# Kernel tuning notes

Measured on AMD Instinct MI355X. Metric: run time of the kernel, lower is better.

## Reference

```python
import jax, jax.numpy as jnp
import numpy as np

B, S, D_IN, D_OUT = 2, 2048, 2048, 2048
NH, NKV = 16, 4
HD = D_OUT // NH          # 128
GS = NH // NKV            # 4


def _rope_tables(seq_len, head_dim, base=10000.0):
    inv = 1.0 / (base ** (np.arange(0, head_dim, 2, dtype=np.float32) / head_dim))
    t = np.arange(seq_len, dtype=np.float32)
    ang = np.outer(t, inv)                       # [S, HD/2]
    ang = np.concatenate([ang, ang], axis=-1)    # [S, HD]
    return jnp.asarray(np.cos(ang)), jnp.asarray(np.sin(ang))


def setup_inputs() -> dict:
    key = jax.random.key(0)
    ks = jax.random.split(key, 5)
    x = jax.random.normal(ks[0], (B, S, D_IN), dtype=jnp.float32)
    Wq = jax.random.normal(ks[1], (D_IN, D_OUT), dtype=jnp.float32) * 0.02
    Wk = jax.random.normal(ks[2], (D_IN, NKV * HD), dtype=jnp.float32) * 0.02
    Wv = jax.random.normal(ks[3], (D_IN, NKV * HD), dtype=jnp.float32) * 0.02
    Wo = jax.random.normal(ks[4], (D_OUT, D_OUT), dtype=jnp.float32) * 0.02
    cos, sin = _rope_tables(S, HD)
    return {"x": x, "Wq": Wq, "Wk": Wk, "Wv": Wv, "Wo": Wo, "cos": cos, "sin": sin}


def _apply_rope(t, cos, sin):
    # t: [b, h, s, hd]; cos/sin: [s, hd]
    hd = t.shape[-1]
    t1, t2 = t[..., : hd // 2], t[..., hd // 2:]
    rot = jnp.concatenate([-t2, t1], axis=-1)
    return t * cos[None, None, :, :] + rot * sin[None, None, :, :]


def reference(x, Wq, Wk, Wv, Wo, cos, sin):
    b, s, _ = x.shape
    q = (x @ Wq).reshape(b, s, NH, HD).transpose(0, 2, 1, 3)    # [b, nh, s, hd]
    k = (x @ Wk).reshape(b, s, NKV, HD).transpose(0, 2, 1, 3)   # [b, nkv, s, hd]
    v = (x @ Wv).reshape(b, s, NKV, HD).transpose(0, 2, 1, 3)
    q = _apply_rope(q, cos, sin)
    k = _apply_rope(k, cos, sin)
    # GQA: repeat_interleave kv heads to match query heads
    k = jnp.repeat(k, GS, axis=1)                               # [b, nh, s, hd]
    v = jnp.repeat(v, GS, axis=1)
    att = jnp.einsum("bhqd,bhkd->bhqk", q, k) / jnp.sqrt(jnp.float32(HD))
    causal = jnp.triu(jnp.ones((s, s), dtype=bool), k=1)         # True above diag
    att = jnp.where(causal[None, None, :, :], -jnp.inf, att)
    att = jax.nn.softmax(att, axis=-1)
    ctx = jnp.einsum("bhqk,bhkd->bhqd", att, v)                  # [b, nh, s, hd]
    ctx = ctx.transpose(0, 2, 1, 3).reshape(b, s, NH * HD)
    return ctx @ Wo
```

## Files before the change

kernel.cpp:

```cpp
#include <hip/hip_runtime.h>

#define B_ 2
#define S_ 2048
#define DIN 2048
#define DOUT 2048
#define NH 16
#define NKV 4
#define HD 128
#define QS3 3072
#define KOFF 2048
#define VOFF 2560
#define SMAX 14.0f
#define NQT 16

typedef __bf16 bf16x8 __attribute__((ext_vector_type(8)));
typedef float f32x4 __attribute__((ext_vector_type(4)));

__device__ inline unsigned short f2bf(float f) {
  union { float f; unsigned int u; } v; v.f = f;
  unsigned int r = v.u + 0x7fffu + ((v.u >> 16) & 1u);
  return (unsigned short)(r >> 16);
}
__device__ inline unsigned short f2bf_trunc(float f) {
  return (unsigned short)(__builtin_bit_cast(unsigned int, f) >> 16);
}
__device__ inline float bf2f(unsigned short h) {
  union { unsigned int u; float f; } v; v.u = ((unsigned int)h) << 16;
  return v.f;
}
#if __has_builtin(__builtin_amdgcn_exp2f)
__device__ inline float exp2_fast(float x) { return __builtin_amdgcn_exp2f(x); }
#else
__device__ inline float exp2_fast(float x) {
  float r;
  asm("v_exp_f32 %0, %1\n\ts_nop 1" : "=v"(r) : "v"(x));
  return r;
}
#endif

__device__ inline void gl_lds16(const void* g, void* l) {
  __builtin_amdgcn_global_load_lds(
      (const __attribute__((address_space(1))) void*)g,
      (__attribute__((address_space(3))) void*)l, 16, 0, 0);
}

template <int N>
__device__ inline float rrot(float v) {
  return __builtin_bit_cast(float,
      __builtin_amdgcn_update_dpp(0, __builtin_bit_cast(int, v), 0x120 | N, 0xF, 0xF, true));
}
__device__ inline float rsum16(float v) {
  v += rrot<1>(v); v += rrot<2>(v); v += rrot<4>(v); v += rrot<8>(v);
  return v;
}

__global__ __launch_bounds__(256) void cast_bf16_k(const float* __restrict__ in,
                                                   unsigned short* __restrict__ out, int n4) {
  int i = blockIdx.x * 256 + threadIdx.x;
  if (i >= n4) return;
  float4 v = ((const float4*)in)[i];
  ushort4 o;
  o.x = f2bf(v.x); o.y = f2bf(v.y); o.z = f2bf(v.z); o.w = f2bf(v.w);
  ((ushort4*)out)[i] = o;
}

__global__ void transpose_cast_k(const float* __restrict__ W, unsigned short* __restrict__ Wt,
                                 int K, int N, float scale) {
  __shared__ float tile[32][33];
  int n0 = blockIdx.x * 32, k0 = blockIdx.y * 32;
  int tx = threadIdx.x, ty = threadIdx.y;
  #pragma unroll
  for (int j = 0; j < 32; j += 8)
    tile[ty + j][tx] = W[(size_t)(k0 + ty + j) * N + n0 + tx];
  __syncthreads();
  #pragma unroll
  for (int j = 0; j < 32; j += 8)
    Wt[(size_t)(n0 + ty + j) * K + k0 + tx] = f2bf(tile[tx][ty + j] * scale);
}

__global__ void transpose_v_k(const unsigned short* __restrict__ QKV,
                              unsigned short* __restrict__ Vt) {
  __shared__ unsigned short t[32][33];
  int c0 = blockIdx.x * 32, s0 = blockIdx.y * 32, b = blockIdx.z;
  int tx = threadIdx.x, ty = threadIdx.y;
  #pragma unroll
  for (int j = 0; j < 32; j += 8)
    t[ty + j][tx] = QKV[(size_t)(b * S_ + s0 + ty + j) * QS3 + VOFF + c0 + tx];
  __syncthreads();
  #pragma unroll
  for (int j = 0; j < 32; j += 8)
    Vt[(size_t)(b * (NKV * HD) + c0 + ty + j) * S_ + s0 + tx] = t[tx][ty + j];
}

template <int OUT_BF16>
__global__ __launch_bounds__(256) void gemm_bt_k(const unsigned short* __restrict__ A,
                                                 const unsigned short* __restrict__ Bt,
                                                 void* __restrict__ Cout,
                                                 int M, int N, int K) {
  __shared__ unsigned short As[128 * 32];
  __shared__ unsigned short Bs[128 * 32];
  int tid = threadIdx.x;
  int lane = tid & 63, wave = tid >> 6;
  int wy = wave >> 1, wx = wave & 1;
  int rowA0 = blockIdx.x * 128, rowB0 = blockIdx.y * 128;
  int m16 = lane & 15, quad = lane >> 4;
  int xq = (m16 >> 1) & 3;
  f32x4 acc[4][4] = {};

  int r0 = tid >> 2, l0 = (tid & 3) ^ ((r0 >> 1) & 3);
  int c1 = 256 + tid;
  int r1 = c1 >> 2, l1 = (c1 & 3) ^ ((r1 >> 1) & 3);
  const unsigned short* pa0 = A  + (size_t)(rowA0 + r0) * K + l0 * 8;
  const unsigned short* pa1 = A  + (size_t)(rowA0 + r1) * K + l1 * 8;
  const unsigned short* pb0 = Bt + (size_t)(rowB0 + r0) * K + l0 * 8;
  const unsigned short* pb1 = Bt + (size_t)(rowB0 + r1) * K + l1 * 8;
  unsigned short* la = As + (tid & 192) * 8;
  unsigned short* lb = Bs + (tid & 192) * 8;

  for (int k0 = 0; k0 < K; k0 += 32) {
    __syncthreads();
    gl_lds16(pa0 + k0, la);
    gl_lds16(pb0 + k0, lb);
    gl_lds16(pa1 + k0, la + 2048);
    gl_lds16(pb1 + k0, lb + 2048);
    __syncthreads();
    bf16x8 af[4], bfr[4];
    #pragma unroll
    for (int i = 0; i < 4; ++i)
      af[i] = *(const bf16x8*)(As + (wy * 64 + i * 16 + m16) * 32 + (quad ^ xq) * 8);
    #pragma unroll
    for (int j = 0; j < 4; ++j)
      bfr[j] = *(const bf16x8*)(Bs + (wx * 64 + j * 16 + m16) * 32 + (quad ^ xq) * 8);
    #pragma unroll
    for (int i = 0; i < 4; ++i)
      #pragma unroll
      for (int j = 0; j < 4; ++j)
        acc[i][j] = __builtin_amdgcn_mfma_f32_16x16x32_bf16(af[i], bfr[j], acc[i][j], 0, 0, 0);
  }

  #pragma unroll
  for (int i = 0; i < 4; ++i) {
    #pragma unroll
    for (int j = 0; j < 4; ++j) {
      int row = rowA0 + wy * 64 + i * 16 + quad * 4;
      int col = rowB0 + wx * 64 + j * 16 + m16;
      #pragma unroll
      for (int r = 0; r < 4; ++r) {
        float v = acc[i][j][r];
        if (OUT_BF16)
          ((unsigned short*)Cout)[(size_t)(row + r) * N + col] = f2bf(v);
        else
          ((float*)Cout)[(size_t)(row + r) * N + col] = v;
      }
    }
  }
}

__global__ __launch_bounds__(256) void rope_k(unsigned short* __restrict__ T,
                                              const float* __restrict__ cosT,
                                              const float* __restrict__ sinT,
                                              int stride, int off, int lognh) {
  int idx = blockIdx.x * 256 + threadIdx.x;
  int d = (idx & 15) * 4;
  int t = idx >> 4;
  int nh = 1 << lognh;
  int h = t & (nh - 1);
  int bs = t >> lognh;
  int s = bs & (S_ - 1);
  unsigned short* p = T + (size_t)bs * stride + off + h * HD;
  ushort4 a = *(ushort4*)(p + d);
  ushort4 bq = *(ushort4*)(p + 64 + d);
  float4 c = *(const float4*)(cosT + s * HD + d);
  float4 sn = *(const float4*)(sinT + s * HD + d);
  ushort4 o1, o2;
  o1.x = f2bf(bf2f(a.x) * c.x - bf2f(bq.x) * sn.x);
  o2.x = f2bf(bf2f(bq.x) * c.x + bf2f(a.x) * sn.x);
  o1.y = f2bf(bf2f(a.y) * c.y - bf2f(bq.y) * sn.y);
  o2.y = f2bf(bf2f(bq.y) * c.y + bf2f(a.y) * sn.y);
  o1.z = f2bf(bf2f(a.z) * c.z - bf2f(bq.z) * sn.z);
  o2.z = f2bf(bf2f(bq.z) * c.z + bf2f(a.z) * sn.z);
  o1.w = f2bf(bf2f(a.w) * c.w - bf2f(bq.w) * sn.w);
  o2.w = f2bf(bf2f(bq.w) * c.w + bf2f(a.w) * sn.w);
  *(ushort4*)(p + d) = o1;
  *(ushort4*)(p + 64 + d) = o2;
}

#define LDP 40
__global__ __launch_bounds__(256) void flash_k(const unsigned short* __restrict__ QKV,
                                               const unsigned short* __restrict__ Vt,
                                               unsigned short* __restrict__ ctx,
                                               unsigned short* __restrict__ Opart,
                                               float* __restrict__ lpart,
                                               int CHUNK, int units_per_bh) {
  __shared__ unsigned short Ks4[4][32 * 128];
  __shared__ unsigned short Vs4[4][128 * 32];
  __shared__ unsigned short Ps[4][32 * LDP];
  int tid = threadIdx.x;
  int lane = tid & 63, w = tid >> 6;
  int m16 = lane & 15, quad = lane >> 4;
  int h = blockIdx.y, b = blockIdx.z;
  int g = h >> 2;

  int u = units_per_bh - 1 - (int)blockIdx.x;
  int qt = 0, prefix = 0, nc = 1;
  for (qt = 0; qt < NQT; ++qt) {
    nc = ((qt + 1) * 128 + CHUNK - 1) / CHUNK;
    if (prefix + nc > u) break;
    prefix += nc;
  }
  int ci = u - prefix;
  bool sole = (nc == 1);
  int kbeg = ci * CHUNK;
  int kend = min(kbeg + CHUNK, (qt + 1) * 128);
  int ntiles = (kend - kbeg) >> 5;
  int unit = (b * NH + h) * units_per_bh + u;

  bf16x8 qf[2][4];
  #pragma unroll
  for (int m = 0; m < 2; ++m) {
    int qrow = qt * 128 + w * 32 + m * 16 + m16;
    const unsigned short* Qp = QKV + (size_t)(b * S_ + qrow) * QS3 + h * HD;
    #pragma unroll
    for (int c = 0; c < 4; ++c) qf[m][c] = *(const bf16x8*)(Qp + c * 32 + quad * 8);
  }

  f32x4 o[2][8] = {};
  float lp[2][4] = {};

  int kxq = m16 & 7;
  int vxq = (m16 >> 1) & 3;

  int krow0 = tid >> 4, kcl0 = (tid & 15) ^ (krow0 & 7);
  int kc1 = 256 + tid;
  int krow1 = kc1 >> 4, kcl1 = (kc1 & 15) ^ (krow1 & 7);
  const unsigned short* kg0 = QKV + (size_t)(b * S_ + krow0) * QS3 + KOFF + g * HD + kcl0 * 8;
  const unsigned short* kg1 = QKV + (size_t)(b * S_ + krow1) * QS3 + KOFF + g * HD + kcl1 * 8;
  int vhd0 = tid >> 2, vcl0 = (tid & 3) ^ ((vhd0 >> 1) & 3);
  int vc1 = 256 + tid;
  int vhd1 = vc1 >> 2, vcl1 = (vc1 & 3) ^ ((vhd1 >> 1) & 3);
  const unsigned short* vg0 = Vt + (size_t)((b * NKV + g) * HD + vhd0) * S_ + vcl0 * 8;
  const unsigned short* vg1 = Vt + (size_t)((b * NKV + g) * HD + vhd1) * S_ + vcl1 * 8;
  int ldsoff = (tid & 192) * 8;
  unsigned short* pw = &Ps[w][0];

  auto stage = [&](int t) {
    int kb = kbeg + t * 32;
    int sl = t & 3;
    gl_lds16(kg0 + (size_t)kb * QS3, Ks4[sl] + ldsoff);
    gl_lds16(kg1 + (size_t)kb * QS3, Ks4[sl] + ldsoff + 2048);
    gl_lds16(vg0 + kb, Vs4[sl] + ldsoff);
    gl_lds16(vg1 + kb, Vs4[sl] + ldsoff + 2048);
  };

  auto qk_tile = [&](const unsigned short* ks, f32x4 (&sf)[2][2]) {
    #pragma unroll
    for (int c = 0; c < 4; ++c)
      #pragma unroll
      for (int f = 0; f < 2; ++f) {
        bf16x8 kf = *(const bf16x8*)(ks + (f * 16 + m16) * 128 + ((c * 4 + quad) ^ kxq) * 8);
        sf[0][f] = __builtin_amdgcn_mfma_f32_16x16x32_bf16(qf[0][c], kf, sf[0][f], 0, 0, 0);
        sf[1][f] = __builtin_amdgcn_mfma_f32_16x16x32_bf16(qf[1][c], kf, sf[1][f], 0, 0, 0);
      }
  };

  auto sm_pv = [&](f32x4 (&sf)[2][2], int kb, const unsigned short* vs) {
    #pragma unroll
    for (int m = 0; m < 2; ++m) {
      int base = qt * 128 + w * 32 + m * 16;
      bool nm = (kb + 31 > base);
      #pragma unroll
      for (int r = 0; r < 4; ++r) {
        float s0 = sf[m][0][r], s1 = sf[m][1][r];
        if (nm) {
          int qr = base + quad * 4 + r;
          if (kb + m16 > qr)      s0 = -1e30f;
          if (kb + 16 + m16 > qr) s1 = -1e30f;
        }
        float p0 = exp2_fast(s0 - SMAX);
        float p1 = exp2_fast(s1 - SMAX);
        lp[m][r] += p0 + p1;
        pw[(m * 16 + quad * 4 + r) * LDP + m16]      = f2bf_trunc(p0);
        pw[(m * 16 + quad * 4 + r) * LDP + 16 + m16] = f2bf_trunc(p1);
      }
    }
    bf16x8 pa0 = *(const bf16x8*)(pw + m16 * LDP + quad * 8);
    bf16x8 pa1 = *(const bf16x8*)(pw + (16 + m16) * LDP + quad * 8);
    #pragma unroll
    for (int nt = 0; nt < 8; ++nt) {
      bf16x8 vf = *(const bf16x8*)(vs + (nt * 16 + m16) * 32 + (quad ^ vxq) * 8);
      o[0][nt] = __builtin_amdgcn_mfma_f32_16x16x32_bf16(pa0, vf, o[0][nt], 0, 0, 0);
      o[1][nt] = __builtin_amdgcn_mfma_f32_16x16x32_bf16(pa1, vf, o[1][nt], 0, 0, 0);
    }
  };

  stage(0);
  stage(1);

  for (int tp = 0; tp < ntiles; tp += 2) {
    __syncthreads();
    if (tp + 2 < ntiles) { stage(tp + 2); stage(tp + 3); }
    int sa = tp & 3, sb = (tp + 1) & 3;
    f32x4 sfa[2][2] = {}, sfb[2][2] = {};
    qk_tile(Ks4[sa], sfa);
    qk_tile(Ks4[sb], sfb);
    sm_pv(sfa, kbeg + tp * 32, Vs4[sa]);
    sm_pv(sfb, kbeg + tp * 32 + 32, Vs4[sb]);
  }

  if (sole) {
    #pragma unroll
    for (int m = 0; m < 2; ++m)
      #pragma unroll
      for (int r = 0; r < 4; ++r) {
        float inv = 1.f / rsum16(lp[m][r]);
        int row = qt * 128 + w * 32 + m * 16 + quad * 4 + r;
        #pragma unroll
        for (int nt = 0; nt < 8; ++nt)
          ctx[(size_t)(b * S_ + row) * DOUT + h * HD + nt * 16 + m16] =
              f2bf(o[m][nt][r] * inv);
      }
  } else {
    unsigned short* Op = Opart + (size_t)unit * 128 * 128;
    #pragma unroll
    for (int m = 0; m < 2; ++m)
      #pragma unroll
      for (int r = 0; r < 4; ++r) {
        int row = w * 32 + m * 16 + quad * 4 + r;
        float ls = rsum16(lp[m][r]);
        if (m16 == 0) lpart[(size_t)unit * 128 + row] = ls;
        #pragma unroll
        for (int nt = 0; nt < 8; ++nt)
          Op[row * 128 + nt * 16 + m16] = f2bf(o[m][nt][r]);
      }
  }
}

__global__ __launch_bounds__(256) void combine_k(const unsigned short* __restrict__ Opart,
                                                 const float* __restrict__ lpart,
                                                 unsigned short* __restrict__ ctx,
                                                 int CHUNK, int units_per_bh) {
  int qt = 4 + blockIdx.x, h = blockIdx.y, b = blockIdx.z;
  int prefix = 0;
  for (int j = 0; j < qt; ++j) prefix += ((j + 1) * 128 + CHUNK - 1) / CHUNK;
  int nc = ((qt + 1) * 128 + CHUNK - 1) / CHUNK;
  int unit0 = (b * NH + h) * units_per_bh + prefix;

  int tid = threadIdx.x;
  int row = tid >> 1, colb = (tid & 1) * 64;
  float denom = 0.f;
  for (int c = 0; c < nc; ++c) denom += lpart[(size_t)(unit0 + c) * 128 + row];
  float inv = 1.f / denom;

  unsigned short* dst = ctx + (size_t)(b * S_ + qt * 128 + row) * DOUT + h * HD + colb;
  for (int j = 0; j < 64; j += 8) {
    float s[8] = {};
    for (int c = 0; c < nc; ++c) {
      const unsigned short* src =
          Opart + (size_t)(unit0 + c) * 128 * 128 + row * 128 + colb + j;
      ushort4 v0 = *(const ushort4*)src;
      ushort4 v1 = *(const ushort4*)(src + 4);
      s[0] += bf2f(v0.x); s[1] += bf2f(v0.y); s[2] += bf2f(v0.z); s[3] += bf2f(v0.w);
      s[4] += bf2f(v1.x); s[5] += bf2f(v1.y); s[6] += bf2f(v1.z); s[7] += bf2f(v1.w);
    }
    ushort4 o0, o1;
    o0.x = f2bf(s[0] * inv); o0.y = f2bf(s[1] * inv);
    o0.z = f2bf(s[2] * inv); o0.w = f2bf(s[3] * inv);
    o1.x = f2bf(s[4] * inv); o1.y = f2bf(s[5] * inv);
    o1.z = f2bf(s[6] * inv); o1.w = f2bf(s[7] * inv);
    *(ushort4*)(dst + j) = o0;
    *(ushort4*)(dst + j + 4) = o1;
  }
}

extern "C" void kernel_launch(void* const* d_in, const int* in_sizes, int n_in,
                              void* d_out, int out_size, void* d_ws, size_t ws_size,
                              hipStream_t stream) {
  const float* x    = (const float*)d_in[0];
  const float* Wq   = (const float*)d_in[1];
  const float* Wk   = (const float*)d_in[2];
  const float* Wv   = (const float*)d_in[3];
  const float* Wo   = (const float*)d_in[4];
  const float* cosT = (const float*)d_in[5];
  const float* sinT = (const float*)d_in[6];

  char* ws = (char*)d_ws;
  size_t off = 0;
  auto alloc = [&](size_t bytes) { char* p = ws + off; off += bytes; return p; };
  unsigned short* xb   = (unsigned short*)alloc((size_t)B_ * S_ * DIN * 2);
  unsigned short* Wqkvt= (unsigned short*)alloc((size_t)QS3 * DIN * 2);
  unsigned short* Wot  = (unsigned short*)alloc((size_t)DOUT * DOUT * 2);
  unsigned short* QKV  = (unsigned short*)alloc((size_t)B_ * S_ * QS3 * 2);
  unsigned short* Vt   = (unsigned short*)alloc((size_t)B_ * NKV * HD * S_ * 2);
  unsigned short* ctx  = xb;

  int CHUNK = 512;
  int upb = 0;
  for (int qt = 0; qt < NQT; ++qt) upb += ((qt + 1) * 128 + CHUNK - 1) / CHUNK;
  size_t part_bytes = (size_t)B_ * NH * upb * 128 * 128 * 2;
  size_t lpart_bytes = (size_t)B_ * NH * upb * 128 * 4;
  bool split = (ws_size >= off + part_bytes + lpart_bytes);
  unsigned short* Opart = nullptr;
  float* lpartp = nullptr;
  if (split) {
    Opart = (unsigned short*)alloc(part_bytes);
    lpartp = (float*)alloc(lpart_bytes);
  } else {
    CHUNK = NQT * 128;
    upb = NQT;
    Opart = (unsigned short*)ws;
    lpartp = (float*)ws;
  }

  int M = B_ * S_;
  const float qscale = 0.08838834764831845f * 1.4426950408889634f;

  int nx4 = B_ * S_ * DIN / 4;
  cast_bf16_k<<<dim3(nx4 / 256), 256, 0, stream>>>(x, xb, nx4);

  transpose_cast_k<<<dim3(DOUT / 32, DIN / 32), dim3(32, 8), 0, stream>>>(Wq, Wqkvt, DIN, DOUT, qscale);
  transpose_cast_k<<<dim3(16, DIN / 32), dim3(32, 8), 0, stream>>>(
      Wk, Wqkvt + (size_t)KOFF * DIN, DIN, NKV * HD, 1.0f);
  transpose_cast_k<<<dim3(16, DIN / 32), dim3(32, 8), 0, stream>>>(
      Wv, Wqkvt + (size_t)VOFF * DIN, DIN, NKV * HD, 1.0f);
  transpose_cast_k<<<dim3(DOUT / 32, DOUT / 32), dim3(32, 8), 0, stream>>>(Wo, Wot, DOUT, DOUT, 1.0f);

  gemm_bt_k<1><<<dim3(M / 128, QS3 / 128), 256, 0, stream>>>(xb, Wqkvt, QKV, M, QS3, DIN);

  rope_k<<<dim3(B_ * S_ * NH * 16 / 256), 256, 0, stream>>>(QKV, cosT, sinT, QS3, 0, 4);
  rope_k<<<dim3(B_ * S_ * NKV * 16 / 256), 256, 0, stream>>>(QKV, cosT, sinT, QS3, KOFF, 2);

  transpose_v_k<<<dim3(16, S_ / 32, B_), dim3(32, 8), 0, stream>>>(QKV, Vt);

  flash_k<<<dim3(upb, NH, B_), 256, 0, stream>>>(QKV, Vt, ctx, Opart, lpartp, CHUNK, upb);
  if (split)
    combine_k<<<dim3(NQT - 4, NH, B_), 256, 0, stream>>>(Opart, lpartp, ctx, CHUNK, upb);

  gemm_bt_k<0><<<dim3(M / 128, DOUT / 128), 256, 0, stream>>>(ctx, Wot, d_out, M, DOUT, DIN);
}
```

Before: 363.0 us.

## Merge prep and post kernels and shrink flash split chunk to 256

Merges the x cast and four weight transpose-casts into one prep kernel, and the two RoPE launches plus the V transpose into one post kernel, cutting kernel launches and tail gaps. The split-KV flash chunk now tries 256 before 512, creating more work units per head for better CU occupancy. It also needs more partial-output workspace and a larger combine pass. The combine start tile is generalised to CHUNK/128.

```diff
diff --git a/kernel.cpp b/kernel.cpp
--- a/kernel.cpp
+++ b/kernel.cpp
@@ -54,120 +54,54 @@
   return v;
 }
 
-__global__ __launch_bounds__(256) void cast_bf16_k(const float* __restrict__ in,
-                                                   unsigned short* __restrict__ out, int n4) {
-  int i = blockIdx.x * 256 + threadIdx.x;
-  if (i >= n4) return;
-  float4 v = ((const float4*)in)[i];
-  ushort4 o;
-  o.x = f2bf(v.x); o.y = f2bf(v.y); o.z = f2bf(v.z); o.w = f2bf(v.w);
-  ((ushort4*)out)[i] = o;
-}
-
-__global__ void transpose_cast_k(const float* __restrict__ W, unsigned short* __restrict__ Wt,
-                                 int K, int N, float scale) {
+__global__ __launch_bounds__(256) void prep_k(const float* __restrict__ x,
+                                              const float* __restrict__ Wq,
+                                              const float* __restrict__ Wk,
+                                              const float* __restrict__ Wv,
+                                              const float* __restrict__ Wo,
+                                              unsigned short* __restrict__ xb,
+                                              unsigned short* __restrict__ Wqkvt,
+                                              unsigned short* __restrict__ Wot,
+                                              float qscale) {
   __shared__ float tile[32][33];
-  int n0 = blockIdx.x * 32, k0 = blockIdx.y * 32;
-  int tx = threadIdx.x, ty = threadIdx.y;
+  int bid = blockIdx.x, tid = threadIdx.x;
+  if (bid < 8192) {
+    int i = bid * 256 + tid;
+    float4 v = ((const float4*)x)[i];
+    ushort4 o;
+    o.x = f2bf(v.x); o.y = f2bf(v.y); o.z = f2bf(v.z); o.w = f2bf(v.w);
+    ((ushort4*)xb)[i] = o;
+    return;
+  }
+  bid -= 8192;
+  const float* W; unsigned short* Wt; int N; float sc;
+  if (bid < 4096)      { W = Wq; Wt = Wqkvt;                        N = 2048; sc = qscale; }
+  else if (bid < 5120) { W = Wk; Wt = Wqkvt + (size_t)KOFF * DIN;   N = 512;  sc = 1.f; bid -= 4096; }
+  else if (bid < 6144) { W = Wv; Wt = Wqkvt + (size_t)VOFF * DIN;   N = 512;  sc = 1.f; bid -= 5120; }
+  else                 { W = Wo; Wt = Wot;                          N = 2048; sc = 1.f; bid -= 6144; }
+  int nx = N >> 5;
+  int n0 = (bid % nx) * 32, k0 = (bid / nx) * 32;
+  int tx = tid & 31, ty = tid >> 5;
   #pragma unroll
   for (int j = 0; j < 32; j += 8)
     tile[ty + j][tx] = W[(size_t)(k0 + ty + j) * N + n0 + tx];
   __syncthreads();
   #pragma unroll
   for (int j = 0; j < 32; j += 8)
-    Wt[(size_t)(n0 + ty + j) * K + k0 + tx] = f2bf(tile[tx][ty + j] * scale);
-}
-
-__global__ void transpose_v_k(const unsigned short* __restrict__ QKV,
-                              unsigned short* __restrict__ Vt) {
-  __shared__ unsigned short t[32][33];
-  int c0 = blockIdx.x * 32, s0 = blockIdx.y * 32, b = blockIdx.z;
-  int tx = threadIdx.x, ty = threadIdx.y;
-  #pragma unroll
-  for (int j = 0; j < 32; j += 8)
-    t[ty + j][tx] = QKV[(size_t)(b * S_ + s0 + ty + j) * QS3 + VOFF + c0 + tx];
-  __syncthreads();
-  #pragma unroll
-  for (int j = 0; j < 32; j += 8)
-    Vt[(size_t)(b * (NKV * HD) + c0 + ty + j) * S_ + s0 + tx] = t[tx][ty + j];
-}
-
-template <int OUT_BF16>
-__global__ __launch_bounds__(256) void gemm_bt_k(const unsigned short* __restrict__ A,
-                                                 const unsigned short* __restrict__ Bt,
-                                                 void* __restrict__ Cout,
-                                                 int M, int N, int K) {
-  __shared__ unsigned short As[128 * 32];
-  __shared__ unsigned short Bs[128 * 32];
-  int tid = threadIdx.x;
-  int lane = tid & 63, wave = tid >> 6;
-  int wy = wave >> 1, wx = wave & 1;
-  int rowA0 = blockIdx.x * 128, rowB0 = blockIdx.y * 128;
-  int m16 = lane & 15, quad = lane >> 4;
-  int xq = (m16 >> 1) & 3;
-  f32x4 acc[4][4] = {};
-
-  int r0 = tid >> 2, l0 = (tid & 3) ^ ((r0 >> 1) & 3);
-  int c1 = 256 + tid;
-  int r1 = c1 >> 2, l1 = (c1 & 3) ^ ((r1 >> 1) & 3);
-  const unsigned short* pa0 = A  + (size_t)(rowA0 + r0) * K + l0 * 8;
-  const unsigned short* pa1 = A  + (size_t)(rowA0 + r1) * K + l1 * 8;
-  const unsigned short* pb0 = Bt + (size_t)(rowB0 + r0) * K + l0 * 8;
-  const unsigned short* pb1 = Bt + (size_t)(rowB0 + r1) * K + l1 * 8;
-  unsigned short* la = As + (tid & 192) * 8;
-  unsigned short* lb = Bs + (tid & 192) * 8;
-
-  for (int k0 = 0; k0 < K; k0 += 32) {
-    __syncthreads();
-    gl_lds16(pa0 + k0, la);
-    gl_lds16(pb0 + k0, lb);
-    gl_lds16(pa1 + k0, la + 2048);
-    gl_lds16(pb1 + k0, lb + 2048);
-    __syncthreads();
-    bf16x8 af[4], bfr[4];
-    #pragma unroll
-    for (int i = 0; i < 4; ++i)
-      af[i] = *(const bf16x8*)(As + (wy * 64 + i * 16 + m16) * 32 + (quad ^ xq) * 8);
-    #pragma unroll
-    for (int j = 0; j < 4; ++j)
-      bfr[j] = *(const bf16x8*)(Bs + (wx * 64 + j * 16 + m16) * 32 + (quad ^ xq) * 8);
-    #pragma unroll
-    for (int i = 0; i < 4; ++i)
-      #pragma unroll
-      for (int j = 0; j < 4; ++j)
-        acc[i][j] = __builtin_amdgcn_mfma_f32_16x16x32_bf16(af[i], bfr[j], acc[i][j], 0, 0, 0);
-  }
-
-  #pragma unroll
-  for (int i = 0; i < 4; ++i) {
-    #pragma unroll
-    for (int j = 0; j < 4; ++j) {
-      int row = rowA0 + wy * 64 + i * 16 + quad * 4;
-      int col = rowB0 + wx * 64 + j * 16 + m16;
-      #pragma unroll
-      for (int r = 0; r < 4; ++r) {
-        float v = acc[i][j][r];
-        if (OUT_BF16)
-          ((unsigned short*)Cout)[(size_t)(row + r) * N + col] = f2bf(v);
-        else
-          ((float*)Cout)[(size_t)(row + r) * N + col] = v;
-      }
-    }
-  }
-}
-
-__global__ __launch_bounds__(256) void rope_k(unsigned short* __restrict__ T,
-                                              const float* __restrict__ cosT,
-                                              const float* __restrict__ sinT,
-                                              int stride, int off, int lognh) {
-  int idx = blockIdx.x * 256 + threadIdx.x;
+    Wt[(size_t)(n0 + ty + j) * DIN + k0 + tx] = f2bf(tile[tx][ty + j] * sc);
+}
+
+__device__ inline void rope_body(unsigned short* __restrict__ T,
+                                 const float* __restrict__ cosT,
+                                 const float* __restrict__ sinT,
+                                 int off, int lognh, int idx) {
   int d = (idx & 15) * 4;
   int t = idx >> 4;
   int nh = 1 << lognh;
   int h = t & (nh - 1);
   int bs = t >> lognh;
   int s = bs & (S_ - 1);
-  unsigned short* p = T + (size_t)bs * stride + off + h * HD;
+  unsigned short* p = T + (size_t)bs * QS3 + off + h * HD;
   ushort4 a = *(ushort4*)(p + d);
   ushort4 bq = *(ushort4*)(p + 64 + d);
   float4 c = *(const float4*)(cosT + s * HD + d);
@@ -183,6 +117,90 @@
   o2.w = f2bf(bf2f(bq.w) * c.w + bf2f(a.w) * sn.w);
   *(ushort4*)(p + d) = o1;
   *(ushort4*)(p + 64 + d) = o2;
+}
+
+__global__ __launch_bounds__(256) void post_k(unsigned short* __restrict__ QKV,
+                                              const float* __restrict__ cosT,
+                                              const float* __restrict__ sinT,
+                                              unsigned short* __restrict__ Vt) {
+  __shared__ unsigned short t[32][33];
+  int bid = blockIdx.x, tid = threadIdx.x;
+  if (bid < 4096) { rope_body(QKV, cosT, sinT, 0, 4, bid * 256 + tid); return; }
+  if (bid < 5120) { rope_body(QKV, cosT, sinT, KOFF, 2, (bid - 4096) * 256 + tid); return; }
+  bid -= 5120;
+  int c0 = (bid & 15) * 32, s0 = ((bid >> 4) & 63) * 32, b = bid >> 10;
+  int tx = tid & 31, ty = tid >> 5;
+  #pragma unroll
+  for (int j = 0; j < 32; j += 8)
+    t[ty + j][tx] = QKV[(size_t)(b * S_ + s0 + ty + j) * QS3 + VOFF + c0 + tx];
+  __syncthreads();
+  #pragma unroll
+  for (int j = 0; j < 32; j += 8)
+    Vt[(size_t)(b * (NKV * HD) + c0 + ty + j) * S_ + s0 + tx] = t[tx][ty + j];
+}
+
+template <int OUT_BF16>
+__global__ __launch_bounds__(256) void gemm_bt_k(const unsigned short* __restrict__ A,
+                                                 const unsigned short* __restrict__ Bt,
+                                                 void* __restrict__ Cout,
+                                                 int M, int N, int K) {
+  __shared__ unsigned short As[128 * 32];
+  __shared__ unsigned short Bs[128 * 32];
+  int tid = threadIdx.x;
+  int lane = tid & 63, wave = tid >> 6;
+  int wy = wave >> 1, wx = wave & 1;
+  int rowA0 = blockIdx.x * 128, rowB0 = blockIdx.y * 128;
+  int m16 = lane & 15, quad = lane >> 4;
+  int xq = (m16 >> 1) & 3;
+  f32x4 acc[4][4] = {};
+
+  int r0 = tid >> 2, l0 = (tid & 3) ^ ((r0 >> 1) & 3);
+  int c1 = 256 + tid;
+  int r1 = c1 >> 2, l1 = (c1 & 3) ^ ((r1 >> 1) & 3);
+  const unsigned short* pa0 = A  + (size_t)(rowA0 + r0) * K + l0 * 8;
+  const unsigned short* pa1 = A  + (size_t)(rowA0 + r1) * K + l1 * 8;
+  const unsigned short* pb0 = Bt + (size_t)(rowB0 + r0) * K + l0 * 8;
+  const unsigned short* pb1 = Bt + (size_t)(rowB0 + r1) * K + l1 * 8;
+  unsigned short* la = As + (tid & 192) * 8;
+  unsigned short* lb = Bs + (tid & 192) * 8;
+
+  for (int k0 = 0; k0 < K; k0 += 32) {
+    __syncthreads();
+    gl_lds16(pa0 + k0, la);
+    gl_lds16(pb0 + k0, lb);
+    gl_lds16(pa1 + k0, la + 2048);
+    gl_lds16(pb1 + k0, lb + 2048);
+    __syncthreads();
+    bf16x8 af[4], bfr[4];
+    #pragma unroll
+    for (int i = 0; i < 4; ++i)
+      af[i] = *(const bf16x8*)(As + (wy * 64 + i * 16 + m16) * 32 + (quad ^ xq) * 8);
+    #pragma unroll
+    for (int j = 0; j < 4; ++j)
+      bfr[j] = *(const bf16x8*)(Bs + (wx * 64 + j * 16 + m16) * 32 + (quad ^ xq) * 8);
+    #pragma unroll
+    for (int i = 0; i < 4; ++i)
+      #pragma unroll
+      for (int j = 0; j < 4; ++j)
+        acc[i][j] = __builtin_amdgcn_mfma_f32_16x16x32_bf16(af[i], bfr[j], acc[i][j], 0, 0, 0);
+  }
+
+  #pragma unroll
+  for (int i = 0; i < 4; ++i) {
+    #pragma unroll
+    for (int j = 0; j < 4; ++j) {
+      int row = rowA0 + wy * 64 + i * 16 + quad * 4;
+      int col = rowB0 + wx * 64 + j * 16 + m16;
+      #pragma unroll
+      for (int r = 0; r < 4; ++r) {
+        float v = acc[i][j][r];
+        if (OUT_BF16)
+          ((unsigned short*)Cout)[(size_t)(row + r) * N + col] = f2bf(v);
+        else
+          ((float*)Cout)[(size_t)(row + r) * N + col] = v;
+      }
+    }
+  }
 }
 
 #define LDP 40
@@ -338,8 +356,8 @@
 __global__ __launch_bounds__(256) void combine_k(const unsigned short* __restrict__ Opart,
                                                  const float* __restrict__ lpart,
                                                  unsigned short* __restrict__ ctx,
-                                                 int CHUNK, int units_per_bh) {
-  int qt = 4 + blockIdx.x, h = blockIdx.y, b = blockIdx.z;
+                                                 int CHUNK, int units_per_bh, int qt0) {
+  int qt = qt0 + blockIdx.x, h = blockIdx.y, b = blockIdx.z;
   int prefix = 0;
   for (int j = 0; j < qt; ++j) prefix += ((j + 1) * 128 + CHUNK - 1) / CHUNK;
   int nc = ((qt + 1) * 128 + CHUNK - 1) / CHUNK;
@@ -393,18 +411,27 @@
   unsigned short* Vt   = (unsigned short*)alloc((size_t)B_ * NKV * HD * S_ * 2);
   unsigned short* ctx  = xb;
 
-  int CHUNK = 512;
-  int upb = 0;
-  for (int qt = 0; qt < NQT; ++qt) upb += ((qt + 1) * 128 + CHUNK - 1) / CHUNK;
-  size_t part_bytes = (size_t)B_ * NH * upb * 128 * 128 * 2;
-  size_t lpart_bytes = (size_t)B_ * NH * upb * 128 * 4;
-  bool split = (ws_size >= off + part_bytes + lpart_bytes);
+  auto upb_for = [](int CH) {
+    int u = 0;
+    for (int qt = 0; qt < NQT; ++qt) u += ((qt + 1) * 128 + CH - 1) / CH;
+    return u;
+  };
+  int CHUNK = 0, upb = 0;
   unsigned short* Opart = nullptr;
   float* lpartp = nullptr;
-  if (split) {
-    Opart = (unsigned short*)alloc(part_bytes);
-    lpartp = (float*)alloc(lpart_bytes);
-  } else {
+  for (int CH : {256, 512}) {
+    int u = upb_for(CH);
+    size_t pb = (size_t)B_ * NH * u * 128 * 128 * 2;
+    size_t lb = (size_t)B_ * NH * u * 128 * 4;
+    if (ws_size >= off + pb + lb) {
+      CHUNK = CH; upb = u;
+      Opart = (unsigned short*)alloc(pb);
+      lpartp = (float*)alloc(lb);
+      break;
+    }
+  }
+  bool split = (CHUNK != 0);
+  if (!split) {
     CHUNK = NQT * 128;
     upb = NQT;
     Opart = (unsigned short*)ws;
@@ -414,26 +441,18 @@
   int M = B_ * S_;
   const float qscale = 0.08838834764831845f * 1.4426950408889634f;
 
-  int nx4 = B_ * S_ * DIN / 4;
-  cast_bf16_k<<<dim3(nx4 / 256), 256, 0, stream>>>(x, xb, nx4);
-
-  transpose_cast_k<<<dim3(DOUT / 32, DIN / 32), dim3(32, 8), 0, stream>>>(Wq, Wqkvt, DIN, DOUT, qscale);
-  transpose_cast_k<<<dim3(16, DIN / 32), dim3(32, 8), 0, stream>>>(
-      Wk, Wqkvt + (size_t)KOFF * DIN, DIN, NKV * HD, 1.0f);
-  transpose_cast_k<<<dim3(16, DIN / 32), dim3(32, 8), 0, stream>>>(
-      Wv, Wqkvt + (size_t)VOFF * DIN, DIN, NKV * HD, 1.0f);
-  transpose_cast_k<<<dim3(DOUT / 32, DOUT / 32), dim3(32, 8), 0, stream>>>(Wo, Wot, DOUT, DOUT, 1.0f);
+  prep_k<<<dim3(18432), 256, 0, stream>>>(x, Wq, Wk, Wv, Wo, xb, Wqkvt, Wot, qscale);
 
   gemm_bt_k<1><<<dim3(M / 128, QS3 / 128), 256, 0, stream>>>(xb, Wqkvt, QKV, M, QS3, DIN);
 
-  rope_k<<<dim3(B_ * S_ * NH * 16 / 256), 256, 0, stream>>>(QKV, cosT, sinT, QS3, 0, 4);
-  rope_k<<<dim3(B_ * S_ * NKV * 16 / 256), 256, 0, stream>>>(QKV, cosT, sinT, QS3, KOFF, 2);
-
-  transpose_v_k<<<dim3(16, S_ / 32, B_), dim3(32, 8), 0, stream>>>(QKV, Vt);
+  post_k<<<dim3(7168), 256, 0, stream>>>(QKV, cosT, sinT, Vt);
 
   flash_k<<<dim3(upb, NH, B_), 256, 0, stream>>>(QKV, Vt, ctx, Opart, lpartp, CHUNK, upb);
-  if (split)
-    combine_k<<<dim3(NQT - 4, NH, B_), 256, 0, stream>>>(Opart, lpartp, ctx, CHUNK, upb);
+
+  if (split) {
+    int qt0 = CHUNK / 128;
+    combine_k<<<dim3(NQT - qt0, NH, B_), 256, 0, stream>>>(Opart, lpartp, ctx, CHUNK, upb, qt0);
+  }
 
   gemm_bt_k<0><<<dim3(M / 128, DOUT / 128), 256, 0, stream>>>(ctx, Wot, d_out, M, DOUT, DIN);
 }
```

Measured after the change: 401.3 us. 1.11x slower.
